# Optimization experiments

Measured on AMD Instinct MI355X. Metric: run time of the kernel, lower is better.

The kernel has to match this reference:

```python
import jax, jax.numpy as jnp
import numpy as np

EPS = 1e-6  # torch.nn.CosineSimilarity eps
P, C, D = 8192, 8192, 256
MAX_ID = 16384


def setup_inputs() -> dict:
    key = jax.random.key(0)
    k1, k2, k3, k4 = jax.random.split(key, 4)
    return {
        "prev_feat": jax.random.normal(k1, (P, D), dtype=jnp.float32),
        "cur_feat": jax.random.normal(k2, (C, D), dtype=jnp.float32),
        "prev_ids": jax.random.randint(k3, (P,), 0, MAX_ID, dtype=jnp.int64),
        "cur_ids": jax.random.randint(k4, (C,), 0, MAX_ID, dtype=jnp.int64),
    }


def _cosine_matrix(prev_feat, cur_feat):
    # torch CosineSimilarity(dim=0): dot / max(||a||*||b||, eps)
    dots = jnp.einsum("pd,cd->pc", prev_feat, cur_feat)  # [P, C]
    n_p = jnp.linalg.norm(prev_feat, axis=1)  # [P]
    n_c = jnp.linalg.norm(cur_feat, axis=1)   # [C]
    denom = jnp.maximum(n_p[:, None] * n_c[None, :], EPS)
    return dots / denom


def _bce_with_logits(logits, labels):
    # mean( max(x,0) - x*y + log(1 + exp(-|x|)) )
    return jnp.mean(
        jnp.maximum(logits, 0.0) - logits * labels + jnp.log1p(jnp.exp(-jnp.abs(logits)))
    )


def reference(prev_feat, cur_feat, prev_ids, cur_ids):
    # previous (tracked) features are detached in the original
    prev_detached = jax.lax.stop_gradient(prev_feat)
    pred_assoc = _cosine_matrix(prev_detached, cur_feat)           # [P, C] logits
    gt_assoc = (prev_ids[:, None] == cur_ids[None, :]).astype(pred_assoc.dtype)
    return _bce_with_logits(pred_assoc, gt_assoc)
```

## Files before the change

### kernel.cpp

```cpp
#include <hip/hip_runtime.h>
#include <hip/hip_bf16.h>

typedef __attribute__((ext_vector_type(4))) float f32x4;
typedef __attribute__((ext_vector_type(2))) float f32x2;
typedef __attribute__((ext_vector_type(4))) int i32x4;
typedef __attribute__((ext_vector_type(8))) int i32x8;

constexpr int P = 8192, C = 8192, D = 256;
constexpr int DB = D / 2;

__device__ __forceinline__ void gload_lds16(const void* g, void* l) {
    __builtin_amdgcn_global_load_lds((const __attribute__((address_space(1))) void*)g,
                                     (__attribute__((address_space(3))) void*)l, 16, 0, 0);
}

__device__ __forceinline__ unsigned int q4(float t) {
    const float a = fabsf(t);
    unsigned int c = (a >= 0.25f) + (a >= 0.75f) + (a >= 1.25f) + (a >= 1.75f)
                   + (a >= 2.5f) + (a >= 3.5f) + (a >= 5.0f);
    return c | (t < 0.f ? 8u : 0u);
}

__global__ __launch_bounds__(256) void prep_kernel(const float* __restrict__ prev,
                                                   const float* __restrict__ cur,
                                                   unsigned char* __restrict__ prevb,
                                                   unsigned char* __restrict__ curb) {
    const int lane = threadIdx.x & 63;
    const int wv = threadIdx.x >> 6;
    const int row = blockIdx.x * 4 + wv;
    const float* src;
    unsigned char* dst;
    int r;
    if (row < P) { src = prev; dst = prevb; r = row; }
    else         { src = cur;  dst = curb;  r = row - P; }
    const float4 v = *(const float4*)(src + (size_t)r * D + lane * 4);
    float ss = v.x * v.x + v.y * v.y + v.z * v.z + v.w * v.w;
#pragma unroll
    for (int off = 32; off; off >>= 1) ss += __shfl_xor(ss, off, 64);
    const float s8 = 8.0f / sqrtf(ss);
    const unsigned int b0 = q4(v.x * s8) | (q4(v.y * s8) << 4);
    const unsigned int b1 = q4(v.z * s8) | (q4(v.w * s8) << 4);
    ((unsigned short*)(dst + (size_t)r * DB))[lane] = (unsigned short)(b0 | (b1 << 8));
}

#define MFMA_SC4(A, B, ACC) \
    __builtin_amdgcn_mfma_scale_f32_16x16x128_f8f6f4( \
        (A), (B), (ACC), 4, 4, 0, 0x7C7C7C7C, 0, 0x7C7C7C7C)

#define SBAR() asm volatile("s_barrier" ::: "memory")

__global__ __attribute__((amdgpu_flat_work_group_size(512, 512), amdgpu_waves_per_eu(2, 2)))
void gemm_bce_kernel(
    const unsigned char* __restrict__ Ab, const unsigned char* __restrict__ Bb,
    const int* __restrict__ pids, const int* __restrict__ cids,
    float* __restrict__ partial) {
    __shared__ unsigned char sA[32768];
    __shared__ unsigned char sB[2][16384];
    __shared__ float wsum[8];

    const int tid = threadIdx.x;
    const int lane = tid & 63;
    const int wv = tid >> 6;
    const int wm = wv >> 2, wn = wv & 3;
    const int fr = lane & 15, fq = lane >> 4;
    const int bid = blockIdx.x;
    const int cslab = (bid & 7) * 1024;
    const int pblock = (bid >> 3) * 256;

    auto stageA = [&]() {
#pragma unroll
        for (int i = 0; i < 4; ++i) {
            const int G = i * 512 + tid;
            const int row = G >> 3, g = G & 7;
            gload_lds16(Ab + (size_t)(pblock + row) * DB + ((g ^ (row & 7)) * 16),
                        &sA[G * 16]);
        }
    };
    auto stageB = [&](int t) {
#pragma unroll
        for (int i = 0; i < 2; ++i) {
            const int G = i * 512 + tid;
            const int col = G >> 3, g = G & 7;
            gload_lds16(Bb + (size_t)(cslab + t * 128 + col) * DB + ((g ^ (col & 7)) * 16),
                        &sB[t & 1][G * 16]);
        }
    };

    int pidp[16];
#pragma unroll
    for (int m = 0; m < 8; ++m)
#pragma unroll
        for (int rp = 0; rp < 2; ++rp) {
            const int base = pblock + wm * 128 + m * 16 + fq * 4 + rp * 2;
            pidp[m * 2 + rp] = (pids[base] & 0xffff) | (pids[base + 1] << 16);
        }
    asm volatile("" ::: "memory");

    stageA();
    stageB(0);
    stageB(1);
    asm volatile("s_waitcnt vmcnt(2)" ::: "memory");
    SBAR();

    i32x8 afr[8][2];
#pragma unroll
    for (int m = 0; m < 8; ++m)
#pragma unroll
        for (int kt = 0; kt < 2; ++kt) {
            const int row = wm * 128 + m * 16 + fr;
            const int g = kt * 4 + fq;
            const i32x4 lo = *(const i32x4*)&sA[row * DB + ((g ^ (row & 7)) * 16)];
            afr[m][kt] = __builtin_shufflevector(lo, lo, 0, 1, 2, 3, 0, 1, 2, 3);
        }

    constexpr float C1 = 0.125f, C2 = -5.2083333e-3f, C3 = 3.4722222e-4f, C4 = -2.6354832e-5f;
    f32x2 sh2 = {0.f, 0.f}, sx2 = {0.f, 0.f};

    for (int t = 0; t < 8; ++t) {
        const unsigned char* pb = &sB[t & 1][0];
        i32x8 bfr[2][2];
#pragma unroll
        for (int n = 0; n < 2; ++n)
#pragma unroll
            for (int kt = 0; kt < 2; ++kt) {
                const int col = wn * 32 + n * 16 + fr;
                const int g = kt * 4 + fq;
                const i32x4 lo = *(const i32x4*)&pb[col * DB + ((g ^ (col & 7)) * 16)];
                bfr[n][kt] = __builtin_shufflevector(lo, lo, 0, 1, 2, 3, 0, 1, 2, 3);
            }

        f32x4 acc[8][2] = {};
        __builtin_amdgcn_s_setprio(1);
#pragma unroll
        for (int kt = 0; kt < 2; ++kt)
#pragma unroll
            for (int m = 0; m < 8; ++m)
#pragma unroll
                for (int n = 0; n < 2; ++n)
                    acc[m][n] = MFMA_SC4(afr[m][kt], bfr[n][kt], acc[m][n]);
        __builtin_amdgcn_s_setprio(0);

        SBAR();
        int cid_r[2];
#pragma unroll
        for (int n = 0; n < 2; ++n)
            cid_r[n] = cids[cslab + t * 128 + wn * 32 + n * 16 + fr];
        if (t < 6) stageB(t + 2);

#pragma unroll
        for (int m = 0; m < 8; ++m)
#pragma unroll
            for (int n = 0; n < 2; ++n)
#pragma unroll
                for (int rp = 0; rp < 2; ++rp) {
                    const f32x2 x = {acc[m][n][rp * 2], acc[m][n][rp * 2 + 1]};
                    const f32x2 t2 = x * x;
                    f32x2 q = t2 * C4 + C3;
                    q = t2 * q + C2;
                    q = t2 * q + C1;
                    sh2 = t2 * q + sh2;
                    const int pp = pidp[m * 2 + rp];
                    const f32x2 cc = {
                        ((pp & 0xffff) == cid_r[n]) ? -0.5f : 0.5f,
                        ((pp >> 16)    == cid_r[n]) ? -0.5f : 0.5f};
                    sx2 = x * cc + sx2;
                }

        if (t < 6)       asm volatile("s_waitcnt vmcnt(2)" ::: "memory");
        else if (t == 6) asm volatile("s_waitcnt vmcnt(0)" ::: "memory");
        if (t < 7) SBAR();
    }

    float lsum = sh2.x + sh2.y + sx2.x + sx2.y;
#pragma unroll
    for (int off = 32; off; off >>= 1) lsum += __shfl_xor(lsum, off, 64);
    if (lane == 0) wsum[wv] = lsum;
    __syncthreads();
    if (tid == 0) {
        float bsum = 0.f;
#pragma unroll
        for (int w = 0; w < 8; ++w) bsum += wsum[w];
        partial[bid] = bsum;
    }
}

__global__ __launch_bounds__(256) void reduce_kernel(const float* __restrict__ part,
                                                     float* __restrict__ out) {
    const int tid = threadIdx.x;
    double s = (double)part[tid];
#pragma unroll
    for (int off = 32; off; off >>= 1) s += __shfl_xor(s, off, 64);
    __shared__ double red[4];
    const int lane = tid & 63, wv = tid >> 6;
    if (lane == 0) red[wv] = s;
    __syncthreads();
    if (tid == 0)
        out[0] = (float)((red[0] + red[1] + red[2] + red[3]) * (1.0 / ((double)P * (double)C))
                         + 0.69314718055994531);
}

extern "C" void kernel_launch(void* const* d_in, const int* in_sizes, int n_in,
                              void* d_out, int out_size, void* d_ws, size_t ws_size,
                              hipStream_t stream) {
    const float* prev_feat = (const float*)d_in[0];
    const float* cur_feat  = (const float*)d_in[1];
    const int* prev_ids    = (const int*)d_in[2];
    const int* cur_ids     = (const int*)d_in[3];
    float* out = (float*)d_out;

    char* ws = (char*)d_ws;
    unsigned char* prevb = (unsigned char*)ws;
    unsigned char* curb  = (unsigned char*)(ws + (size_t)P * DB);
    float* partial = (float*)(ws + (size_t)(P + C) * DB);

    prep_kernel<<<(P + C) / 4, 256, 0, stream>>>(prev_feat, cur_feat, prevb, curb);
    gemm_bce_kernel<<<256, 512, 0, stream>>>(prevb, curb, prev_ids, cur_ids, partial);
    reduce_kernel<<<1, 256, 0, stream>>>(partial, out);
}
```

Baseline: 34.70 us.

## Preload all B tiles into LDS up front, removing per-tile barriers

Replaces the double-buffered B pipeline with a single up-front load of seven B tiles into a larger LDS allocation. The eighth tile reuses the A buffer once the A fragments sit in registers. The main loop then runs without barriers or waitcnt handshakes. The block-level reduction is also removed: each wave writes its own partial and the reduce kernel sums 2048 values. The cost is about 144KB of LDS per block and a long serial wait on all loads before any compute starts, so loads no longer overlap with MFMA work inside a block.

```diff
diff --git a/kernel.cpp b/kernel.cpp
--- a/kernel.cpp
+++ b/kernel.cpp
@@ -47,16 +47,13 @@
     __builtin_amdgcn_mfma_scale_f32_16x16x128_f8f6f4( \
         (A), (B), (ACC), 4, 4, 0, 0x7C7C7C7C, 0, 0x7C7C7C7C)
 
-#define SBAR() asm volatile("s_barrier" ::: "memory")
-
 __global__ __attribute__((amdgpu_flat_work_group_size(512, 512), amdgpu_waves_per_eu(2, 2)))
 void gemm_bce_kernel(
     const unsigned char* __restrict__ Ab, const unsigned char* __restrict__ Bb,
     const int* __restrict__ pids, const int* __restrict__ cids,
     float* __restrict__ partial) {
     __shared__ unsigned char sA[32768];
-    __shared__ unsigned char sB[2][16384];
-    __shared__ float wsum[8];
+    __shared__ unsigned char sB[7][16384];
 
     const int tid = threadIdx.x;
     const int lane = tid & 63;
@@ -76,13 +73,13 @@
                         &sA[G * 16]);
         }
     };
-    auto stageB = [&](int t) {
+    auto stageB = [&](int t, unsigned char* dst) {
 #pragma unroll
         for (int i = 0; i < 2; ++i) {
             const int G = i * 512 + tid;
             const int col = G >> 3, g = G & 7;
             gload_lds16(Bb + (size_t)(cslab + t * 128 + col) * DB + ((g ^ (col & 7)) * 16),
-                        &sB[t & 1][G * 16]);
+                        dst + G * 16);
         }
     };
 
@@ -94,13 +91,11 @@
             const int base = pblock + wm * 128 + m * 16 + fq * 4 + rp * 2;
             pidp[m * 2 + rp] = (pids[base] & 0xffff) | (pids[base + 1] << 16);
         }
-    asm volatile("" ::: "memory");
 
     stageA();
-    stageB(0);
-    stageB(1);
-    asm volatile("s_waitcnt vmcnt(2)" ::: "memory");
-    SBAR();
+#pragma unroll
+    for (int t = 0; t < 7; ++t) stageB(t, &sB[t][0]);
+    __syncthreads();
 
     i32x8 afr[8][2];
 #pragma unroll
@@ -112,12 +107,13 @@
             const i32x4 lo = *(const i32x4*)&sA[row * DB + ((g ^ (row & 7)) * 16)];
             afr[m][kt] = __builtin_shufflevector(lo, lo, 0, 1, 2, 3, 0, 1, 2, 3);
         }
+    __syncthreads();
+    stageB(7, &sA[0]);
 
     constexpr float C1 = 0.125f, C2 = -5.2083333e-3f, C3 = 3.4722222e-4f, C4 = -2.6354832e-5f;
     f32x2 sh2 = {0.f, 0.f}, sx2 = {0.f, 0.f};
 
-    for (int t = 0; t < 8; ++t) {
-        const unsigned char* pb = &sB[t & 1][0];
+    auto tileBody = [&](int t, const unsigned char* pb) {
         i32x8 bfr[2][2];
 #pragma unroll
         for (int n = 0; n < 2; ++n)
@@ -128,7 +124,6 @@
                 const i32x4 lo = *(const i32x4*)&pb[col * DB + ((g ^ (col & 7)) * 16)];
                 bfr[n][kt] = __builtin_shufflevector(lo, lo, 0, 1, 2, 3, 0, 1, 2, 3);
             }
-
         f32x4 acc[8][2] = {};
         __builtin_amdgcn_s_setprio(1);
 #pragma unroll
@@ -140,13 +135,10 @@
                     acc[m][n] = MFMA_SC4(afr[m][kt], bfr[n][kt], acc[m][n]);
         __builtin_amdgcn_s_setprio(0);
 
-        SBAR();
         int cid_r[2];
 #pragma unroll
         for (int n = 0; n < 2; ++n)
             cid_r[n] = cids[cslab + t * 128 + wn * 32 + n * 16 + fr];
-        if (t < 6) stageB(t + 2);
-
 #pragma unroll
         for (int m = 0; m < 8; ++m)
 #pragma unroll
@@ -165,29 +157,25 @@
                         ((pp >> 16)    == cid_r[n]) ? -0.5f : 0.5f};
                     sx2 = x * cc + sx2;
                 }
-
-        if (t < 6)       asm volatile("s_waitcnt vmcnt(2)" ::: "memory");
-        else if (t == 6) asm volatile("s_waitcnt vmcnt(0)" ::: "memory");
-        if (t < 7) SBAR();
-    }
+    };
+
+#pragma unroll 1
+    for (int t = 0; t < 7; ++t) tileBody(t, &sB[t][0]);
+
+    __syncthreads();
+    tileBody(7, &sA[0]);
 
     float lsum = sh2.x + sh2.y + sx2.x + sx2.y;
 #pragma unroll
     for (int off = 32; off; off >>= 1) lsum += __shfl_xor(lsum, off, 64);
-    if (lane == 0) wsum[wv] = lsum;
-    __syncthreads();
-    if (tid == 0) {
-        float bsum = 0.f;
-#pragma unroll
-        for (int w = 0; w < 8; ++w) bsum += wsum[w];
-        partial[bid] = bsum;
-    }
+    if (lane == 0) partial[bid * 8 + wv] = lsum;
 }
 
 __global__ __launch_bounds__(256) void reduce_kernel(const float* __restrict__ part,
                                                      float* __restrict__ out) {
     const int tid = threadIdx.x;
-    double s = (double)part[tid];
+    double s = 0.0;
+    for (int i = tid; i < 2048; i += 256) s += (double)part[i];
 #pragma unroll
     for (int off = 32; off; off >>= 1) s += __shfl_xor(s, off, 64);
     __shared__ double red[4];
```

Result: no change. 34.26 us (median of 2 runs) (-1.3%).
